# Kernel optimization log

Measured on AMD Instinct MI355X. Metric: run time of the kernel, lower is better.

The kernel has to match this reference:

```python
import jax, jax.numpy as jnp
import numpy as np

B, C, H, W = 8, 256, 64, 64
RED = 16

def setup_inputs() -> dict:
    key = jax.random.key(0)
    ks = jax.random.split(key, 10)
    s = 0.05
    return {
        "x": jax.random.normal(ks[0], (B, C, H, W), jnp.float32),
        "ca_w1": jax.random.normal(ks[1], (C // RED, C), jnp.float32) * s,
        "ca_w2": jax.random.normal(ks[2], (C, C // RED), jnp.float32) * s,
        "q_w": jax.random.normal(ks[3], (C // RED, C), jnp.float32) * s,
        "q_b": jax.random.normal(ks[4], (C // RED,), jnp.float32) * s,
        "k_w": jax.random.normal(ks[5], (C // RED, C), jnp.float32) * s,
        "k_b": jax.random.normal(ks[6], (C // RED,), jnp.float32) * s,
        "v_w": jax.random.normal(ks[7], (C, C), jnp.float32) * s,
        "v_b": jax.random.normal(ks[8], (C,), jnp.float32) * s,
        "gamma": jax.random.normal(ks[9], (1,), jnp.float32) * s,
    }

def _cbam(x, ca_w1, ca_w2, q_w, q_b, k_w, k_b, v_w, v_b, gamma):
    # ---- Channel attention (squeeze-excite with avg+max pooling) ----
    avg = jnp.mean(x, axis=(2, 3))          # [B, C]
    mx = jnp.max(x, axis=(2, 3))            # [B, C]
    def fc(s):
        h = jax.nn.relu(jnp.einsum('rc,bc->br', ca_w1, s))
        return jnp.einsum('cr,br->bc', ca_w2, h)
    gate = jax.nn.sigmoid(fc(avg) + fc(mx))[:, :, None, None]
    x = x * gate
    # ---- Spatial (non-local) attention ----
    b, c, h, w = x.shape
    hw = h * w
    xf = x.reshape(b, c, hw)                          # [B, C, HW]
    q = jnp.einsum('rc,bcn->brn', q_w, xf) + q_b[None, :, None]   # [B, C/r, HW]
    k = jnp.einsum('rc,bcn->brn', k_w, xf) + k_b[None, :, None]
    v = jnp.einsum('oc,bcn->bon', v_w, xf) + v_b[None, :, None]   # [B, C, HW]
    attn = jax.nn.softmax(jnp.einsum('bri,brj->bij', q, k), axis=-1)  # [B, HW, HW]
    out = jnp.einsum('bcj,bij->bci', v, attn).reshape(b, c, h, w)
    return gamma[0] * out + x

def reference(x, ca_w1, ca_w2, q_w, q_b, k_w, k_b, v_w, v_b, gamma):
    return _cbam(x, ca_w1, ca_w2, q_w, q_b, k_w, k_b, v_w, v_b, gamma)
```

## Files before the change

kernel.cpp:

```cpp
#include <hip/hip_runtime.h>
#include <hip/hip_bf16.h>
#include <math.h>

#define BB 8
#define CCH 256
#define HWN 4096
#define RR 16

typedef __attribute__((ext_vector_type(8))) short short8;
typedef __attribute__((ext_vector_type(4))) float f32x4;

static __device__ __forceinline__ unsigned short f2bf(float x) {
    union { float f; unsigned u; } v; v.f = x;
    return (unsigned short)((v.u + 0x8000u) >> 16);
}

__global__ __launch_bounds__(256) void k_pool(const float* __restrict__ x,
                                              float* __restrict__ avgp,
                                              float* __restrict__ maxp,
                                              const float* __restrict__ vw,
                                              const float* __restrict__ qw,
                                              const float* __restrict__ kw,
                                              unsigned short* __restrict__ Wb) {
    int bc = blockIdx.x;
    int t = threadIdx.x;
    if (bc < 288) {
        int idx = bc * 256 + t;
        int m = idx >> 8, c = idx & 255;
        float v;
        if (m < 256) v = vw[idx];
        else if (m < 272) v = qw[(m - 256) * 256 + c];
        else v = kw[(m - 272) * 256 + c];
        Wb[idx] = f2bf(v);
    }
    const float4* p = (const float4*)(x + (size_t)bc * HWN);
    float s = 0.f, m = -INFINITY;
#pragma unroll
    for (int i = 0; i < 4; ++i) {
        float4 v = p[t + 256 * i];
        s += v.x + v.y + v.z + v.w;
        m = fmaxf(m, fmaxf(fmaxf(v.x, v.y), fmaxf(v.z, v.w)));
    }
    for (int off = 32; off; off >>= 1) {
        s += __shfl_down(s, off);
        m = fmaxf(m, __shfl_down(m, off));
    }
    __shared__ float ss[4], sm[4];
    int wid = t >> 6;
    if ((t & 63) == 0) { ss[wid] = s; sm[wid] = m; }
    __syncthreads();
    if (t == 0) {
        float S = ss[0] + ss[1] + ss[2] + ss[3];
        float M = fmaxf(fmaxf(sm[0], sm[1]), fmaxf(sm[2], sm[3]));
        avgp[bc] = S * (1.f / (float)HWN);
        maxp[bc] = M;
    }
}

__global__ __launch_bounds__(256) void k_gate(const float* __restrict__ avgp,
                                              const float* __restrict__ maxp,
                                              const float* __restrict__ w1,
                                              const float* __restrict__ w2,
                                              float* __restrict__ gate) {
    int b = blockIdx.x, t = threadIdx.x;
    __shared__ float sa[CCH], sx[CCH], sh[32];
    sa[t] = avgp[b * CCH + t];
    sx[t] = maxp[b * CCH + t];
    __syncthreads();
    if (t < 32) {
        int r = t & 15;
        const float* src = (t < 16) ? sa : sx;
        float h = 0.f;
        for (int c = 0; c < CCH; ++c) h += w1[r * CCH + c] * src[c];
        sh[t] = fmaxf(h, 0.f);
    }
    __syncthreads();
    float g = 0.f;
#pragma unroll
    for (int r = 0; r < RR; ++r) g += w2[t * RR + r] * (sh[r] + sh[16 + r]);
    gate[b * CCH + t] = 1.f / (1.f + __expf(-g));
}

__global__ __launch_bounds__(256) void k_proj(const float* __restrict__ x,
                                              const float* __restrict__ gate,
                                              const unsigned short* __restrict__ Wb,
                                              const float* __restrict__ vb,
                                              const float* __restrict__ qb,
                                              const float* __restrict__ kb,
                                              unsigned short* __restrict__ qT,
                                              unsigned short* __restrict__ kT,
                                              unsigned short* __restrict__ vB) {
    int b = blockIdx.x & 7;
    int n0 = (blockIdx.x >> 3) << 6;
    int t = threadIdx.x;
    int w = t >> 6, l = t & 63, quad = l >> 4, ln = l & 15;

    __shared__ __align__(16) unsigned short xs_t[64][72];
    __shared__ __align__(16) unsigned short vtile[256 * 72];
    __shared__ float qk_s[32][66];

    const f32x4 zf = {0.f, 0.f, 0.f, 0.f};
    f32x4 acc[18];
#pragma unroll
    for (int mt = 0; mt < 18; ++mt) acc[mt] = zf;

    for (int cc = 0; cc < 4; ++cc) {
        __syncthreads();
#pragma unroll
        for (int it = 0; it < 4; ++it) {
            int idx = it * 256 + t;
            int cl = idx >> 4, nq = idx & 15;
            int c = cc * 64 + cl;
            float g = gate[b * CCH + c];
            float4 v = *(const float4*)(x + (((size_t)(b * CCH + c)) << 12) + n0 + nq * 4);
            xs_t[nq * 4 + 0][cl] = f2bf(v.x * g);
            xs_t[nq * 4 + 1][cl] = f2bf(v.y * g);
            xs_t[nq * 4 + 2][cl] = f2bf(v.z * g);
            xs_t[nq * 4 + 3][cl] = f2bf(v.w * g);
        }
        __syncthreads();

        short8 bfrag[2];
#pragma unroll
        for (int kc = 0; kc < 2; ++kc)
            bfrag[kc] = *(const short8*)&xs_t[w * 16 + ln][kc * 32 + quad * 8];

#pragma unroll
        for (int mt = 0; mt < 18; ++mt) {
#pragma unroll
            for (int kc = 0; kc < 2; ++kc) {
                short8 af = *(const short8*)(Wb + ((size_t)(mt * 16 + ln)) * 256 + cc * 64 + kc * 32 + quad * 8);
                acc[mt] = __builtin_amdgcn_mfma_f32_16x16x32_bf16(af, bfrag[kc], acc[mt], 0, 0, 0);
            }
        }
    }

#pragma unroll
    for (int mt = 0; mt < 16; ++mt) {
#pragma unroll
        for (int r = 0; r < 4; ++r) {
            int m = mt * 16 + quad * 4 + r;
            vtile[m * 72 + w * 16 + ln] = f2bf(acc[mt][r] + vb[m]);
        }
    }
#pragma unroll
    for (int r = 0; r < 4; ++r) {
        qk_s[quad * 4 + r][w * 16 + ln] = acc[16][r];
        qk_s[16 + quad * 4 + r][w * 16 + ln] = acc[17][r];
    }
    __syncthreads();

    {
        unsigned short* vBp = vB + (((size_t)b) << 20);
        int c = t;
#pragma unroll
        for (int Q = 0; Q < 8; ++Q) {
            short8 v8 = *(const short8*)(vtile + c * 72 + Q * 8);
            *(short8*)(vBp + ((size_t)((((n0 >> 3) + Q) << 8) + c) << 3)) = v8;
        }
    }
    if (t < 128) {
        int isK = t >> 6;
        int n = t & 63;
        const float* bias = isK ? kb : qb;
        unsigned u32[8];
#pragma unroll
        for (int j = 0; j < 8; ++j) {
            unsigned lo = f2bf(qk_s[isK * 16 + 2 * j][n] + bias[2 * j]);
            unsigned hi = f2bf(qk_s[isK * 16 + 2 * j + 1][n] + bias[2 * j + 1]);
            u32[j] = lo | (hi << 16);
        }
        unsigned short* dst = (isK ? kT : qT) + ((size_t)(b * HWN + n0 + n)) * RR;
        uint4 d0 = {u32[0], u32[1], u32[2], u32[3]};
        uint4 d1 = {u32[4], u32[5], u32[6], u32[7]};
        ((uint4*)dst)[0] = d0;
        ((uint4*)dst)[1] = d1;
    }
}

__global__ __launch_bounds__(512, 4) void k_attn(const unsigned short* __restrict__ qT,
                                                 const unsigned short* __restrict__ kT,
                                                 const unsigned short* __restrict__ vB,
                                                 const float* __restrict__ x,
                                                 const float* __restrict__ gate,
                                                 const float* __restrict__ gamma,
                                                 float* __restrict__ out) {
    int b = blockIdx.x & 7;
    int i0 = (blockIdx.x >> 3) << 5;
    int t = threadIdx.x;
    int w = __builtin_amdgcn_readfirstlane(t >> 6);
    int l = t & 63;
    int quad = l >> 4, ln = l & 15;
    int isub = w & 1, jsub = w >> 1;
    int c0 = w * 32;

    __shared__ __align__(16) unsigned short p_lds[2][2048];
    __shared__ float l_s[4][36];

    const short8 zs = {0, 0, 0, 0, 0, 0, 0, 0};
    const f32x4 zf = {0.f, 0.f, 0.f, 0.f};

    short8 bq = zs;
    if (quad < 2)
        bq = *(const short8*)(qT + (((size_t)(b * HWN + i0 + isub * 16 + ln)) << 4) + (quad << 3));

    f32x4 acc[2][2];
#pragma unroll
    for (int cs = 0; cs < 2; ++cs)
#pragma unroll
        for (int is = 0; is < 2; ++is) acc[cs][is] = zf;
    float lsum = 0.f;

    const float c1 = 1.44269504f;
    const float c0e = -11.5415603f;

    const unsigned short* kb_u = kT + ((size_t)(b * HWN)) * RR;
    const int kln = ((jsub * 16 + ln) << 4) + (quad << 3);
    const unsigned short* vb_u = vB + (((size_t)b) << 20) + ((size_t)c0 << 3);
    int vln[4];
#pragma unroll
    for (int ks = 0; ks < 2; ++ks)
#pragma unroll
        for (int cs = 0; cs < 2; ++cs)
            vln[ks * 2 + cs] = (((ks * 4 + quad) << 8) + cs * 16 + ln) << 3;

    int soff = ((jsub * 2 + (quad >> 1)) * 32 + isub * 16 + ln) * 8 + (quad & 1) * 4;
    int rbase = quad * 256 + ln * 8;

    short8 akA = zs, akB = zs;
    short8 avA[4], avB[4];

    auto load_ak = [&](short8& ak, int j0) {
        if (quad < 2) ak = *(const short8*)(kb_u + ((j0 << 4) + kln));
    };
    auto load_av = [&](short8 (&av)[4], int j0) {
        const unsigned short* vp = vb_u + (j0 << 8);
#pragma unroll
        for (int u = 0; u < 4; ++u) av[u] = *(const short8*)(vp + vln[u]);
    };

    load_ak(akA, 0);
    load_av(avA, 0);

    auto step = [&](short8& akC, short8 (&avC)[4], short8& akN, short8 (&avN)[4],
                    unsigned short* pbuf, int j0n, bool pf) {
        f32x4 sf = __builtin_amdgcn_mfma_f32_16x16x32_bf16(akC, bq, zf, 0, 0, 0);

        float p0 = exp2f(fmaf(sf[0], c1, c0e));
        float p1 = exp2f(fmaf(sf[1], c1, c0e));
        float p2 = exp2f(fmaf(sf[2], c1, c0e));
        float p3 = exp2f(fmaf(sf[3], c1, c0e));
        lsum += (p0 + p1) + (p2 + p3);
        uint2 pk;
        asm("v_cvt_pk_bf16_f32 %0, %1, %2" : "=v"(pk.x) : "v"(p0), "v"(p1));
        asm("v_cvt_pk_bf16_f32 %0, %1, %2" : "=v"(pk.y) : "v"(p2), "v"(p3));
        *(uint2*)(pbuf + soff) = pk;

        __syncthreads();

        if (pf) { load_ak(akN, j0n); load_av(avN, j0n); }

        __builtin_amdgcn_s_setprio(1);
#pragma unroll
        for (int ks = 0; ks < 2; ++ks) {
            short8 bp[2];
#pragma unroll
            for (int is = 0; is < 2; ++is)
                bp[is] = *(const short8*)(pbuf + rbase + ks * 1024 + is * 128);
#pragma unroll
            for (int cs = 0; cs < 2; ++cs)
#pragma unroll
                for (int is = 0; is < 2; ++is)
                    acc[cs][is] = __builtin_amdgcn_mfma_f32_16x16x32_bf16(avC[ks * 2 + cs], bp[is], acc[cs][is], 0, 0, 0);
        }
        __builtin_amdgcn_s_setprio(0);
    };

    for (int jt2 = 0; jt2 < 32; ++jt2) {
        int j0 = jt2 << 7;
        step(akA, avA, akB, avB, &p_lds[0][0], j0 + 64, true);
        step(akB, avB, akA, avA, &p_lds[1][0], (jt2 < 31) ? (j0 + 128) : 0, jt2 < 31);
    }

    lsum += __shfl_xor(lsum, 16, 64);
    lsum += __shfl_xor(lsum, 32, 64);
    if (l < 16) l_s[jsub][isub * 16 + l] = lsum;
    __syncthreads();

    float g = gamma[0];
    float rinv[2];
#pragma unroll
    for (int is = 0; is < 2; ++is) {
        int i = is * 16 + ln;
        float lf = (l_s[0][i] + l_s[1][i]) + (l_s[2][i] + l_s[3][i]);
        rinv[is] = g / lf;
    }

#pragma unroll
    for (int cs = 0; cs < 2; ++cs) {
#pragma unroll
        for (int r = 0; r < 4; ++r) {
            int c = c0 + cs * 16 + quad * 4 + r;
            float gc = gate[b * CCH + c];
            size_t rowoff = (((size_t)(b * CCH + c)) << 12) + i0;
            float* po = out + rowoff;
            const float* px = x + rowoff;
#pragma unroll
            for (int is = 0; is < 2; ++is) {
                int idx = is * 16 + ln;
                po[idx] = acc[cs][is][r] * rinv[is] + px[idx] * gc;
            }
        }
    }
}

extern "C" void kernel_launch(void* const* d_in, const int* in_sizes, int n_in,
                              void* d_out, int out_size, void* d_ws, size_t ws_size,
                              hipStream_t stream) {
    const float* x = (const float*)d_in[0];
    const float* w1 = (const float*)d_in[1];
    const float* w2 = (const float*)d_in[2];
    const float* qw = (const float*)d_in[3];
    const float* qb = (const float*)d_in[4];
    const float* kw = (const float*)d_in[5];
    const float* kb = (const float*)d_in[6];
    const float* vw = (const float*)d_in[7];
    const float* vb = (const float*)d_in[8];
    const float* gamma = (const float*)d_in[9];
    float* out = (float*)d_out;
    char* ws = (char*)d_ws;

    float* avgp = (float*)(ws);
    float* maxp = (float*)(ws + 8192);
    float* gate = (float*)(ws + 16384);
    unsigned short* Wb = (unsigned short*)(ws + 24576);
    unsigned short* qT = (unsigned short*)(ws + 24576 + 147456);
    unsigned short* kT = (unsigned short*)(ws + 24576 + 147456 + 1048576);
    unsigned short* vB = (unsigned short*)(ws + 24576 + 147456 + 2097152);

    k_pool<<<2048, 256, 0, stream>>>(x, avgp, maxp, vw, qw, kw, Wb);
    k_gate<<<8, 256, 0, stream>>>(avgp, maxp, w1, w2, gate);
    k_proj<<<512, 256, 0, stream>>>(x, gate, Wb, vb, qb, kb, qT, kT, vB);
    k_attn<<<1024, 512, 0, stream>>>(qT, kT, vB, x, gate, gamma, out);
}
```

Baseline: 252.0 us.

## Process two key tiles per barrier with quad-buffered P in LDS

```diff
diff --git a/kernel.cpp b/kernel.cpp
--- a/kernel.cpp
+++ b/kernel.cpp
@@ -194,7 +194,7 @@
     int isub = w & 1, jsub = w >> 1;
     int c0 = w * 32;
 
-    __shared__ __align__(16) unsigned short p_lds[2][2048];
+    __shared__ __align__(16) unsigned short p_lds[4][2048];
     __shared__ float l_s[4][36];
 
     const short8 zs = {0, 0, 0, 0, 0, 0, 0, 0};
@@ -240,12 +240,11 @@
     };
 
     load_ak(akA, 0);
+    load_ak(akB, 64);
     load_av(avA, 0);
-
-    auto step = [&](short8& akC, short8 (&avC)[4], short8& akN, short8 (&avN)[4],
-                    unsigned short* pbuf, int j0n, bool pf) {
-        f32x4 sf = __builtin_amdgcn_mfma_f32_16x16x32_bf16(akC, bq, zf, 0, 0, 0);
-
+    load_av(avB, 64);
+
+    auto finish_s = [&](const f32x4& sf, unsigned short* pbuf) {
         float p0 = exp2f(fmaf(sf[0], c1, c0e));
         float p1 = exp2f(fmaf(sf[1], c1, c0e));
         float p2 = exp2f(fmaf(sf[2], c1, c0e));
@@ -255,12 +254,9 @@
         asm("v_cvt_pk_bf16_f32 %0, %1, %2" : "=v"(pk.x) : "v"(p0), "v"(p1));
         asm("v_cvt_pk_bf16_f32 %0, %1, %2" : "=v"(pk.y) : "v"(p2), "v"(p3));
         *(uint2*)(pbuf + soff) = pk;
-
-        __syncthreads();
-
-        if (pf) { load_ak(akN, j0n); load_av(avN, j0n); }
-
-        __builtin_amdgcn_s_setprio(1);
+    };
+
+    auto pv = [&](const short8 (&av)[4], const unsigned short* pbuf) {
 #pragma unroll
         for (int ks = 0; ks < 2; ++ks) {
             short8 bp[2];
@@ -271,15 +267,29 @@
             for (int cs = 0; cs < 2; ++cs)
 #pragma unroll
                 for (int is = 0; is < 2; ++is)
-                    acc[cs][is] = __builtin_amdgcn_mfma_f32_16x16x32_bf16(avC[ks * 2 + cs], bp[is], acc[cs][is], 0, 0, 0);
-        }
-        __builtin_amdgcn_s_setprio(0);
+                    acc[cs][is] = __builtin_amdgcn_mfma_f32_16x16x32_bf16(av[ks * 2 + cs], bp[is], acc[cs][is], 0, 0, 0);
+        }
     };
 
-    for (int jt2 = 0; jt2 < 32; ++jt2) {
-        int j0 = jt2 << 7;
-        step(akA, avA, akB, avB, &p_lds[0][0], j0 + 64, true);
-        step(akB, avB, akA, avA, &p_lds[1][0], (jt2 < 31) ? (j0 + 128) : 0, jt2 < 31);
+    for (int jt = 0; jt < 32; ++jt) {
+        unsigned short* pb0 = &p_lds[(jt & 1) * 2 + 0][0];
+        unsigned short* pb1 = &p_lds[(jt & 1) * 2 + 1][0];
+
+        f32x4 sf0 = __builtin_amdgcn_mfma_f32_16x16x32_bf16(akA, bq, zf, 0, 0, 0);
+        f32x4 sf1 = __builtin_amdgcn_mfma_f32_16x16x32_bf16(akB, bq, zf, 0, 0, 0);
+        finish_s(sf0, pb0);
+        finish_s(sf1, pb1);
+
+        __syncthreads();
+
+        bool pf = jt < 31;
+        int j0n = (jt + 1) << 7;
+        if (pf) { load_ak(akA, j0n); load_ak(akB, j0n + 64); }
+
+        pv(avA, pb0);
+        if (pf) load_av(avA, j0n);
+        pv(avB, pb1);
+        if (pf) load_av(avB, j0n + 64);
     }
 
     lsum += __shfl_xor(lsum, 16, 64);
```

Result: no change. 250.9 us (-0.4%).
